# Performance work log

Hardware: AMD Instinct MI355X
Metric: run time of the kernel (lower is better)

## Reference

```python
import jax, jax.numpy as jnp
import numpy as np

OUT_H, OUT_W = 7, 7
SPATIAL_SCALE = 0.125
SAMPLING_RATIO = 2


def setup_inputs() -> dict:
    key = jax.random.key(0)
    k1, k2, k3, k4 = jax.random.split(key, 4)
    inputs = jax.random.normal(k1, (2, 100, 100, 256), dtype=jnp.float32)
    # boxes in image coords (stride-8 feature over ~800px image): x0,y0,x1,y1
    xy0 = jax.random.uniform(k2, (1024, 2), minval=0.0, maxval=600.0)
    wh = jax.random.uniform(k3, (1024, 2), minval=8.0, maxval=200.0)
    boxes = jnp.concatenate([xy0, xy0 + wh], axis=1).astype(jnp.float32)
    box_inds = jax.random.randint(k4, (1024,), 0, 2, dtype=jnp.int32)
    return {"inputs": inputs, "boxes": boxes, "box_inds": box_inds}


def _roi_align(inputs, boxes, box_inds):
    """aligned=True ROIAlign: crop_and_resize at oversampled grid + avg pool.

    Sample coordinate (per aligned=True transform + tf.crop_and_resize):
      x_j = x0*scale + spacing_w*(j+0.5) - 0.5, spacing_w = w_box*scale/crop_w
    Out-of-range samples get extrapolation_value=0 (TF semantics).
    """
    N, H, W, C = inputs.shape
    B = boxes.shape[0]
    ch, cw = OUT_H * SAMPLING_RATIO, OUT_W * SAMPLING_RATIO

    sb = boxes * SPATIAL_SCALE
    x0, y0, x1, y1 = sb[:, 0], sb[:, 1], sb[:, 2], sb[:, 3]
    sw = (x1 - x0) / cw  # [B]
    sh = (y1 - y0) / ch
    xs = x0[:, None] + sw[:, None] * (jnp.arange(cw, dtype=sb.dtype) + 0.5) - 0.5  # [B,cw]
    ys = y0[:, None] + sh[:, None] * (jnp.arange(ch, dtype=sb.dtype) + 0.5) - 0.5  # [B,ch]

    yl = jnp.floor(ys)
    xl = jnp.floor(xs)
    ty = ys - yl  # [B,ch]
    tx = xs - xl  # [B,cw]
    yli = jnp.clip(yl, 0, H - 1).astype(jnp.int32)
    yhi = jnp.clip(yl + 1, 0, H - 1).astype(jnp.int32)
    xli = jnp.clip(xl, 0, W - 1).astype(jnp.int32)
    xhi = jnp.clip(xl + 1, 0, W - 1).astype(jnp.int32)

    b = box_inds[:, None, None]

    def g(yy, xx):  # gather -> [B,ch,cw,C]
        return inputs[b, yy[:, :, None], xx[:, None, :], :]

    txe = tx[:, None, :, None]
    top = g(yli, xli) * (1.0 - txe) + g(yli, xhi) * txe
    bot = g(yhi, xli) * (1.0 - txe) + g(yhi, xhi) * txe
    tye = ty[:, :, None, None]
    out = top * (1.0 - tye) + bot * tye  # [B,ch,cw,C]

    valid = ((ys >= 0) & (ys <= H - 1))[:, :, None] & ((xs >= 0) & (xs <= W - 1))[:, None, :]
    out = jnp.where(valid[..., None], out, 0.0)

    # avg_pool2d kernel=stride=SAMPLING_RATIO (SAME==VALID since exact multiple)
    out = out.reshape(B, OUT_H, SAMPLING_RATIO, OUT_W, SAMPLING_RATIO, C).mean(axis=(2, 4))
    return out  # [B, OUT_H, OUT_W, C]


def reference(inputs, boxes, box_inds):
    return _roi_align(inputs, boxes, box_inds)
```

## Files before the change

### kernel.cpp

```cpp
#include <hip/hip_runtime.h>


constexpr int   H_IN  = 100;
constexpr int   W_IN  = 100;
constexpr int   C_IN  = 256;
constexpr int   OUT_H = 7;
constexpr int   OUT_W = 7;
constexpr int   SR    = 2;
constexpr int   NPIX  = OUT_H * OUT_W;
constexpr int   NBOX  = 1024;
constexpr float SCALE = 0.125f;

typedef float f32x4 __attribute__((ext_vector_type(4)));

__global__ __launch_bounds__(1024) void sort_boxes_kernel(
    const float* __restrict__ boxes,
    const int*   __restrict__ box_inds,
    int*         __restrict__ perm)
{
    const int tid  = threadIdx.x;
    const int wave = tid >> 6;
    const int lane = tid & 63;

    const float y0 = boxes[tid * 4 + 1] * SCALE;
    const float y1 = boxes[tid * 4 + 3] * SCALE;
    const float cy = 0.5f * (y0 + y1);
    int band = (int)(cy * (1.0f / 25.0f));
    band = min(max(band, 0), 3);
    const int bin = box_inds[tid] * 4 + band;

    __shared__ int whist[16][8];
    __shared__ int wbase[16][8];

    int wrank = 0;
    const unsigned long long ltmask = (lane == 63) ? ~0ull >> 1
                                                   : (1ull << lane) - 1;
#pragma unroll
    for (int k = 0; k < 8; ++k) {
        const unsigned long long bal = __ballot(bin == k);
        if (bin == k) wrank = __popcll(bal & ltmask);
        if (lane == 0) whist[wave][k] = __popcll(bal);
    }
    __syncthreads();

    if (tid == 0) {
        int acc = 0;
        for (int k = 0; k < 8; ++k)
            for (int w = 0; w < 16; ++w) {
                wbase[w][k] = acc;
                acc += whist[w][k];
            }
    }
    __syncthreads();

    perm[wbase[wave][bin] + wrank] = tid;
}

template<int NR, int NC>
__device__ __forceinline__ f32x4 gather(const float* __restrict__ base,
                                        const int* ro, const int* co,
                                        const float* wr, const float* wc,
                                        int c4)
{
    f32x4 v[NR * NC];
#pragma unroll
    for (int i = 0; i < NR; ++i)
#pragma unroll
        for (int j = 0; j < NC; ++j)
            v[i * NC + j] = *(const f32x4*)(base + (size_t)((ro[i] + co[j]) * C_IN + c4));

    f32x4 acc = {0.f, 0.f, 0.f, 0.f};
#pragma unroll
    for (int i = 0; i < NR; ++i)
#pragma unroll
        for (int j = 0; j < NC; ++j)
            acc += v[i * NC + j] * (wr[i] * wc[j]);
    return acc;
}

__device__ __forceinline__ int merge_dim(float s0, float s1, int LIM,
                                         int* idx, float* w)
{
    const float f0 = floorf(s0);
    const float f1 = floorf(s1);
    const float t0 = s0 - f0;
    const float t1 = s1 - f1;
    const float va = (s0 >= 0.0f && s0 <= (float)(LIM - 1)) ? 1.0f : 0.0f;
    const float vb = (s1 >= 0.0f && s1 <= (float)(LIM - 1)) ? 1.0f : 0.0f;
    const int i0 = (int)f0;
    const int i1 = (int)f1;

    int n;
    if (i1 == i0) {
        n = 2;
        idx[0] = i0;     w[0] = va * (1.0f - t0) + vb * (1.0f - t1);
        idx[1] = i0 + 1; w[1] = va * t0 + vb * t1;
    } else if (i1 == i0 + 1) {
        n = 3;
        idx[0] = i0;     w[0] = va * (1.0f - t0);
        idx[1] = i0 + 1; w[1] = va * t0 + vb * (1.0f - t1);
        idx[2] = i0 + 2; w[2] = vb * t1;
    } else {
        n = 4;
        idx[0] = i0;     w[0] = va * (1.0f - t0);
        idx[1] = i0 + 1; w[1] = va * t0;
        idx[2] = i1;     w[2] = vb * (1.0f - t1);
        idx[3] = i1 + 1; w[3] = vb * t1;
    }
#pragma unroll
    for (int k = 0; k < 4; ++k)
        idx[k] = min(max(idx[k], 0), LIM - 1);
    return n;
}

__global__ __launch_bounds__(256) void roi_align_kernel(
    const float* __restrict__ inputs,
    const float* __restrict__ boxes,
    const int*   __restrict__ box_inds,
    const int*   __restrict__ perm,
    float*       __restrict__ out)
{
    const int tid  = threadIdx.x;
    const int lane = tid & 63;
    const int sub  = tid >> 6;

    const int nchunk = gridDim.x >> 3;
    const int lbid   = (blockIdx.x & 7) * nchunk + (blockIdx.x >> 3);
    const int p      = lbid * 4 + sub;

    const int bs  = p / NPIX;
    const int b   = perm[bs];
    const int rem = p - bs * NPIX;
    const int oy  = rem / OUT_W;
    const int ox  = rem - oy * OUT_W;

    const float x0 = boxes[b * 4 + 0] * SCALE;
    const float y0 = boxes[b * 4 + 1] * SCALE;
    const float x1 = boxes[b * 4 + 2] * SCALE;
    const float y1 = boxes[b * 4 + 3] * SCALE;
    const float sw = (x1 - x0) * (1.0f / (OUT_W * SR));
    const float sh = (y1 - y0) * (1.0f / (OUT_H * SR));
    const int   n  = box_inds[b];

    const float* base = inputs + (size_t)n * (H_IN * W_IN * C_IN);
    const int c4 = lane * 4;

    const float ys0 = y0 + sh * ((float)(oy * SR) + 0.5f) - 0.5f;
    const float ys1 = ys0 + sh;
    int   ridx[4]; float wr[4];
    const int nr = merge_dim(ys0, ys1, H_IN, ridx, wr);
#pragma unroll
    for (int k = 0; k < 4; ++k) ridx[k] *= W_IN;

    const float xs0 = x0 + sw * ((float)(ox * SR) + 0.5f) - 0.5f;
    const float xs1 = xs0 + sw;
    int   cidx[4]; float wc[4];
    const int nc = merge_dim(xs0, xs1, W_IN, cidx, wc);

    const int sel = __builtin_amdgcn_readfirstlane((nr - 2) * 3 + (nc - 2));

    f32x4 acc;
    switch (sel) {
        case 0: acc = gather<2, 2>(base, ridx, cidx, wr, wc, c4); break;
        case 1: acc = gather<2, 3>(base, ridx, cidx, wr, wc, c4); break;
        case 2: acc = gather<2, 4>(base, ridx, cidx, wr, wc, c4); break;
        case 3: acc = gather<3, 2>(base, ridx, cidx, wr, wc, c4); break;
        case 4: acc = gather<3, 3>(base, ridx, cidx, wr, wc, c4); break;
        case 5: acc = gather<3, 4>(base, ridx, cidx, wr, wc, c4); break;
        case 6: acc = gather<4, 2>(base, ridx, cidx, wr, wc, c4); break;
        case 7: acc = gather<4, 3>(base, ridx, cidx, wr, wc, c4); break;
        default: acc = gather<4, 4>(base, ridx, cidx, wr, wc, c4); break;
    }

    acc *= 0.25f;

    float* op = out + (size_t)b * (NPIX * C_IN) + (size_t)rem * C_IN + c4;
    __builtin_nontemporal_store(acc, (f32x4*)op);
}

extern "C" void kernel_launch(void* const* d_in, const int* in_sizes, int n_in,
                              void* d_out, int out_size, void* d_ws, size_t ws_size,
                              hipStream_t stream) {
    const float* inputs   = (const float*)d_in[0];
    const float* boxes    = (const float*)d_in[1];
    const int*   box_inds = (const int*)d_in[2];
    float*       out      = (float*)d_out;
    int*         perm     = (int*)d_ws;

    sort_boxes_kernel<<<1, NBOX, 0, stream>>>(boxes, box_inds, perm);

    const int npix_total = NBOX * NPIX;
    const int blocks     = npix_total / 4;
    roi_align_kernel<<<blocks, 256, 0, stream>>>(inputs, boxes, box_inds, perm, out);
}
```

Measured before the change: 31.78 us.

## Process half a box per block with shared per-row/column sample tables

Each block now handles half of one box (about 25 output pixels) rather than 4 arbitrary pixels. Fourteen threads compute the row and column offsets and weights once into LDS, and each wave then loops over its pixels. This removes the redundant per-pixel box loads and merge_dim work and cuts the grid from about 12.5K blocks to 2048. The trade-off is fewer blocks, a __syncthreads, and per-wave loops of uneven length, which may hurt latency hiding on the gather loads.

```diff
diff --git a/kernel.cpp b/kernel.cpp
--- a/kernel.cpp
+++ b/kernel.cpp
@@ -6,7 +6,6 @@
 constexpr int   C_IN  = 256;
 constexpr int   OUT_H = 7;
 constexpr int   OUT_W = 7;
-constexpr int   SR    = 2;
 constexpr int   NPIX  = OUT_H * OUT_W;
 constexpr int   NBOX  = 1024;
 constexpr float SCALE = 0.125f;
@@ -54,28 +53,6 @@
     __syncthreads();
 
     perm[wbase[wave][bin] + wrank] = tid;
-}
-
-template<int NR, int NC>
-__device__ __forceinline__ f32x4 gather(const float* __restrict__ base,
-                                        const int* ro, const int* co,
-                                        const float* wr, const float* wc,
-                                        int c4)
-{
-    f32x4 v[NR * NC];
-#pragma unroll
-    for (int i = 0; i < NR; ++i)
-#pragma unroll
-        for (int j = 0; j < NC; ++j)
-            v[i * NC + j] = *(const f32x4*)(base + (size_t)((ro[i] + co[j]) * C_IN + c4));
-
-    f32x4 acc = {0.f, 0.f, 0.f, 0.f};
-#pragma unroll
-    for (int i = 0; i < NR; ++i)
-#pragma unroll
-        for (int j = 0; j < NC; ++j)
-            acc += v[i * NC + j] * (wr[i] * wc[j]);
-    return acc;
 }
 
 __device__ __forceinline__ int merge_dim(float s0, float s1, int LIM,
@@ -95,11 +72,14 @@
         n = 2;
         idx[0] = i0;     w[0] = va * (1.0f - t0) + vb * (1.0f - t1);
         idx[1] = i0 + 1; w[1] = va * t0 + vb * t1;
+        idx[2] = i0;     w[2] = 0.0f;
+        idx[3] = i0;     w[3] = 0.0f;
     } else if (i1 == i0 + 1) {
         n = 3;
         idx[0] = i0;     w[0] = va * (1.0f - t0);
         idx[1] = i0 + 1; w[1] = va * t0 + vb * (1.0f - t1);
         idx[2] = i0 + 2; w[2] = vb * t1;
+        idx[3] = i0;     w[3] = 0.0f;
     } else {
         n = 4;
         idx[0] = i0;     w[0] = va * (1.0f - t0);
@@ -113,7 +93,29 @@
     return n;
 }
 
-__global__ __launch_bounds__(256) void roi_align_kernel(
+template<int NR, int NC>
+__device__ __forceinline__ f32x4 gather(const float* __restrict__ base,
+                                        const int* ro, const int* co,
+                                        const float* wr, const float* wc,
+                                        int c4)
+{
+    f32x4 v[NR * NC];
+#pragma unroll
+    for (int i = 0; i < NR; ++i)
+#pragma unroll
+        for (int j = 0; j < NC; ++j)
+            v[i * NC + j] = *(const f32x4*)(base + (size_t)(ro[i] + co[j] + c4));
+
+    f32x4 acc = {0.f, 0.f, 0.f, 0.f};
+#pragma unroll
+    for (int i = 0; i < NR; ++i)
+#pragma unroll
+        for (int j = 0; j < NC; ++j)
+            acc += v[i * NC + j] * (wr[i] * wc[j]);
+    return acc;
+}
+
+__global__ __launch_bounds__(256, 4) void roi_align_kernel(
     const float* __restrict__ inputs,
     const float* __restrict__ boxes,
     const int*   __restrict__ box_inds,
@@ -122,60 +124,98 @@
 {
     const int tid  = threadIdx.x;
     const int lane = tid & 63;
-    const int sub  = tid >> 6;
+    const int wv   = tid >> 6;
 
     const int nchunk = gridDim.x >> 3;
     const int lbid   = (blockIdx.x & 7) * nchunk + (blockIdx.x >> 3);
-    const int p      = lbid * 4 + sub;
-
-    const int bs  = p / NPIX;
-    const int b   = perm[bs];
-    const int rem = p - bs * NPIX;
-    const int oy  = rem / OUT_W;
-    const int ox  = rem - oy * OUT_W;
-
-    const float x0 = boxes[b * 4 + 0] * SCALE;
-    const float y0 = boxes[b * 4 + 1] * SCALE;
-    const float x1 = boxes[b * 4 + 2] * SCALE;
-    const float y1 = boxes[b * 4 + 3] * SCALE;
-    const float sw = (x1 - x0) * (1.0f / (OUT_W * SR));
-    const float sh = (y1 - y0) * (1.0f / (OUT_H * SR));
-    const int   n  = box_inds[b];
+    const int bs     = lbid >> 1;
+    const int h      = lbid & 1;
+
+    const int b = __builtin_amdgcn_readfirstlane(perm[bs]);
+    const int n = __builtin_amdgcn_readfirstlane(box_inds[b]);
+
+    __shared__ int4   s_roff[OUT_H];
+    __shared__ float4 s_rw[OUT_H];
+    __shared__ int4   s_coff[OUT_W];
+    __shared__ float4 s_cw[OUT_W];
+    __shared__ int    s_nr[OUT_H];
+    __shared__ int    s_nc[OUT_W];
+
+    if (tid < 14) {
+        const float bx0 = boxes[b * 4 + 0] * SCALE;
+        const float by0 = boxes[b * 4 + 1] * SCALE;
+        const float bx1 = boxes[b * 4 + 2] * SCALE;
+        const float by1 = boxes[b * 4 + 3] * SCALE;
+        const float sw  = (bx1 - bx0) * (1.0f / 14.0f);
+        const float sh  = (by1 - by0) * (1.0f / 14.0f);
+
+        int   idx[4];
+        float wgt[4];
+        if (tid < 7) {
+            const int   oy = tid;
+            const float s0 = by0 + sh * ((float)(oy * 2) + 0.5f) - 0.5f;
+            const int   nr = merge_dim(s0, s0 + sh, H_IN, idx, wgt);
+            int4 off; float4 wq;
+#pragma unroll
+            for (int k = 0; k < 4; ++k) {
+                ((int*)&off)[k]   = idx[k] * (W_IN * C_IN);
+                ((float*)&wq)[k]  = wgt[k] * 0.25f;
+            }
+            s_roff[oy] = off; s_rw[oy] = wq; s_nr[oy] = nr;
+        } else {
+            const int   ox = tid - 7;
+            const float s0 = bx0 + sw * ((float)(ox * 2) + 0.5f) - 0.5f;
+            const int   nc = merge_dim(s0, s0 + sw, W_IN, idx, wgt);
+            int4 off; float4 wq;
+#pragma unroll
+            for (int k = 0; k < 4; ++k) {
+                ((int*)&off)[k]   = idx[k] * C_IN;
+                ((float*)&wq)[k]  = wgt[k];
+            }
+            s_coff[ox] = off; s_cw[ox] = wq; s_nc[ox] = nc;
+        }
+    }
+    __syncthreads();
 
     const float* base = inputs + (size_t)n * (H_IN * W_IN * C_IN);
-    const int c4 = lane * 4;
-
-    const float ys0 = y0 + sh * ((float)(oy * SR) + 0.5f) - 0.5f;
-    const float ys1 = ys0 + sh;
-    int   ridx[4]; float wr[4];
-    const int nr = merge_dim(ys0, ys1, H_IN, ridx, wr);
-#pragma unroll
-    for (int k = 0; k < 4; ++k) ridx[k] *= W_IN;
-
-    const float xs0 = x0 + sw * ((float)(ox * SR) + 0.5f) - 0.5f;
-    const float xs1 = xs0 + sw;
-    int   cidx[4]; float wc[4];
-    const int nc = merge_dim(xs0, xs1, W_IN, cidx, wc);
-
-    const int sel = __builtin_amdgcn_readfirstlane((nr - 2) * 3 + (nc - 2));
-
-    f32x4 acc;
-    switch (sel) {
-        case 0: acc = gather<2, 2>(base, ridx, cidx, wr, wc, c4); break;
-        case 1: acc = gather<2, 3>(base, ridx, cidx, wr, wc, c4); break;
-        case 2: acc = gather<2, 4>(base, ridx, cidx, wr, wc, c4); break;
-        case 3: acc = gather<3, 2>(base, ridx, cidx, wr, wc, c4); break;
-        case 4: acc = gather<3, 3>(base, ridx, cidx, wr, wc, c4); break;
-        case 5: acc = gather<3, 4>(base, ridx, cidx, wr, wc, c4); break;
-        case 6: acc = gather<4, 2>(base, ridx, cidx, wr, wc, c4); break;
-        case 7: acc = gather<4, 3>(base, ridx, cidx, wr, wc, c4); break;
-        default: acc = gather<4, 4>(base, ridx, cidx, wr, wc, c4); break;
-    }
-
-    acc *= 0.25f;
-
-    float* op = out + (size_t)b * (NPIX * C_IN) + (size_t)rem * C_IN + c4;
-    __builtin_nontemporal_store(acc, (f32x4*)op);
+    const int    c4   = lane * 4;
+    const int    start = h * 25;
+    const int    pend  = h ? NPIX : 25;
+
+    for (int k = 0; k < 7; ++k) {
+        const int pix = start + wv + 4 * k;
+        if (pix >= pend) break;
+        const int oy = (pix * 37) >> 8;
+        const int ox = pix - oy * 7;
+
+        int4   roI = s_roff[oy];
+        float4 rwV = s_rw[oy];
+        int4   coI = s_coff[ox];
+        float4 cwV = s_cw[ox];
+        const int* ro   = (const int*)&roI;
+        const float* wr = (const float*)&rwV;
+        const int* co   = (const int*)&coI;
+        const float* wc = (const float*)&cwV;
+
+        const int sel = __builtin_amdgcn_readfirstlane(
+            (s_nr[oy] - 2) * 3 + (s_nc[ox] - 2));
+
+        f32x4 acc;
+        switch (sel) {
+            case 0: acc = gather<2, 2>(base, ro, co, wr, wc, c4); break;
+            case 1: acc = gather<2, 3>(base, ro, co, wr, wc, c4); break;
+            case 2: acc = gather<2, 4>(base, ro, co, wr, wc, c4); break;
+            case 3: acc = gather<3, 2>(base, ro, co, wr, wc, c4); break;
+            case 4: acc = gather<3, 3>(base, ro, co, wr, wc, c4); break;
+            case 5: acc = gather<3, 4>(base, ro, co, wr, wc, c4); break;
+            case 6: acc = gather<4, 2>(base, ro, co, wr, wc, c4); break;
+            case 7: acc = gather<4, 3>(base, ro, co, wr, wc, c4); break;
+            default: acc = gather<4, 4>(base, ro, co, wr, wc, c4); break;
+        }
+
+        float* op = out + ((size_t)b * NPIX + pix) * C_IN + c4;
+        __builtin_nontemporal_store(acc, (f32x4*)op);
+    }
 }
 
 extern "C" void kernel_launch(void* const* d_in, const int* in_sizes, int n_in,
@@ -188,8 +228,5 @@
     int*         perm     = (int*)d_ws;
 
     sort_boxes_kernel<<<1, NBOX, 0, stream>>>(boxes, box_inds, perm);
-
-    const int npix_total = NBOX * NPIX;
-    const int blocks     = npix_total / 4;
-    roi_align_kernel<<<blocks, 256, 0, stream>>>(inputs, boxes, box_inds, perm, out);
-}
+    roi_align_kernel<<<NBOX * 2, 256, 0, stream>>>(inputs, boxes, box_inds, perm, out);
+}
```

Measured after the change: 33.25 us. 4.6% more time.

## Precompute per-box row/column sample offsets and weights in a separate meta kernel

Applied to the files above, without the earlier changes.

Adds a meta_kernel that computes, for each sorted box slot, the 7 row and 7 column merged sample offsets, weights and tap counts, and stores them as 32-byte records in workspace. The main gather kernel then loads two records per output pixel instead of doing box loads, floor, merge and index math per wavefront. Batch offset and the 1/4 average are folded into the row offsets and weights, and the tap count is packed into the low bits of the first offset. This adds a third kernel launch and a workspace round trip in exchange for a leaner gather kernel.

```diff
diff --git a/kernel.cpp b/kernel.cpp
--- a/kernel.cpp
+++ b/kernel.cpp
@@ -6,12 +6,16 @@
 constexpr int   C_IN  = 256;
 constexpr int   OUT_H = 7;
 constexpr int   OUT_W = 7;
-constexpr int   SR    = 2;
 constexpr int   NPIX  = OUT_H * OUT_W;
 constexpr int   NBOX  = 1024;
 constexpr float SCALE = 0.125f;
 
 typedef float f32x4 __attribute__((ext_vector_type(4)));
+
+struct Meta { int4 off; float4 w; };
+
+constexpr int RMETA_OFF = 4096;
+constexpr int CMETA_OFF = 4096 + 7168 * 32;
 
 __global__ __launch_bounds__(1024) void sort_boxes_kernel(
     const float* __restrict__ boxes,
@@ -54,28 +58,6 @@
     __syncthreads();
 
     perm[wbase[wave][bin] + wrank] = tid;
-}
-
-template<int NR, int NC>
-__device__ __forceinline__ f32x4 gather(const float* __restrict__ base,
-                                        const int* ro, const int* co,
-                                        const float* wr, const float* wc,
-                                        int c4)
-{
-    f32x4 v[NR * NC];
-#pragma unroll
-    for (int i = 0; i < NR; ++i)
-#pragma unroll
-        for (int j = 0; j < NC; ++j)
-            v[i * NC + j] = *(const f32x4*)(base + (size_t)((ro[i] + co[j]) * C_IN + c4));
-
-    f32x4 acc = {0.f, 0.f, 0.f, 0.f};
-#pragma unroll
-    for (int i = 0; i < NR; ++i)
-#pragma unroll
-        for (int j = 0; j < NC; ++j)
-            acc += v[i * NC + j] * (wr[i] * wc[j]);
-    return acc;
 }
 
 __device__ __forceinline__ int merge_dim(float s0, float s1, int LIM,
@@ -95,11 +77,14 @@
         n = 2;
         idx[0] = i0;     w[0] = va * (1.0f - t0) + vb * (1.0f - t1);
         idx[1] = i0 + 1; w[1] = va * t0 + vb * t1;
+        idx[2] = i0;     w[2] = 0.0f;
+        idx[3] = i0;     w[3] = 0.0f;
     } else if (i1 == i0 + 1) {
         n = 3;
         idx[0] = i0;     w[0] = va * (1.0f - t0);
         idx[1] = i0 + 1; w[1] = va * t0 + vb * (1.0f - t1);
         idx[2] = i0 + 2; w[2] = vb * t1;
+        idx[3] = i0;     w[3] = 0.0f;
     } else {
         n = 4;
         idx[0] = i0;     w[0] = va * (1.0f - t0);
@@ -113,68 +98,125 @@
     return n;
 }
 
-__global__ __launch_bounds__(256) void roi_align_kernel(
-    const float* __restrict__ inputs,
+__global__ __launch_bounds__(256) void meta_kernel(
     const float* __restrict__ boxes,
     const int*   __restrict__ box_inds,
     const int*   __restrict__ perm,
+    Meta*        __restrict__ rmeta,
+    Meta*        __restrict__ cmeta)
+{
+    const int t = blockIdx.x * 256 + threadIdx.x;
+    if (t >= NBOX * 14) return;
+    const int slot = t / 14;
+    const int d    = t - slot * 14;
+
+    const int b = perm[slot];
+    const int n = box_inds[b];
+
+    const float bx0 = boxes[b * 4 + 0] * SCALE;
+    const float by0 = boxes[b * 4 + 1] * SCALE;
+    const float bx1 = boxes[b * 4 + 2] * SCALE;
+    const float by1 = boxes[b * 4 + 3] * SCALE;
+    const float sw  = (bx1 - bx0) * (1.0f / 14.0f);
+    const float sh  = (by1 - by0) * (1.0f / 14.0f);
+
+    int idx[4]; float wgt[4];
+    Meta m;
+    if (d < 7) {
+        const float s0 = by0 + sh * ((float)(d * 2) + 0.5f) - 0.5f;
+        const int   nr = merge_dim(s0, s0 + sh, H_IN, idx, wgt);
+#pragma unroll
+        for (int k = 0; k < 4; ++k) {
+            ((int*)&m.off)[k]  = n * (H_IN * W_IN * C_IN) + idx[k] * (W_IN * C_IN);
+            ((float*)&m.w)[k]  = wgt[k] * 0.25f;
+        }
+        m.off.x |= (nr - 2);
+        rmeta[slot * 7 + d] = m;
+    } else {
+        const int   ox = d - 7;
+        const float s0 = bx0 + sw * ((float)(ox * 2) + 0.5f) - 0.5f;
+        const int   nc = merge_dim(s0, s0 + sw, W_IN, idx, wgt);
+#pragma unroll
+        for (int k = 0; k < 4; ++k) {
+            ((int*)&m.off)[k]  = idx[k] * C_IN;
+            ((float*)&m.w)[k]  = wgt[k];
+        }
+        m.off.x |= (nc - 2);
+        cmeta[slot * 7 + ox] = m;
+    }
+}
+
+template<int NR, int NC>
+__device__ __forceinline__ f32x4 gather(const float* __restrict__ base,
+                                        const int* ro, const int* co,
+                                        const float* wr, const float* wc,
+                                        int c4)
+{
+    f32x4 v[NR * NC];
+#pragma unroll
+    for (int i = 0; i < NR; ++i)
+#pragma unroll
+        for (int j = 0; j < NC; ++j)
+            v[i * NC + j] = *(const f32x4*)(base + (size_t)(ro[i] + co[j] + c4));
+
+    f32x4 acc = {0.f, 0.f, 0.f, 0.f};
+#pragma unroll
+    for (int i = 0; i < NR; ++i)
+#pragma unroll
+        for (int j = 0; j < NC; ++j)
+            acc += v[i * NC + j] * (wr[i] * wc[j]);
+    return acc;
+}
+
+__global__ __launch_bounds__(256) void roi_align_kernel(
+    const float* __restrict__ inputs,
+    const int*   __restrict__ perm,
+    const Meta*  __restrict__ rmeta,
+    const Meta*  __restrict__ cmeta,
     float*       __restrict__ out)
 {
-    const int tid  = threadIdx.x;
-    const int lane = tid & 63;
-    const int sub  = tid >> 6;
+    const int lane = threadIdx.x & 63;
+    const int sub  = __builtin_amdgcn_readfirstlane(threadIdx.x >> 6);
 
     const int nchunk = gridDim.x >> 3;
     const int lbid   = (blockIdx.x & 7) * nchunk + (blockIdx.x >> 3);
     const int p      = lbid * 4 + sub;
 
     const int bs  = p / NPIX;
-    const int b   = perm[bs];
     const int rem = p - bs * NPIX;
-    const int oy  = rem / OUT_W;
-    const int ox  = rem - oy * OUT_W;
-
-    const float x0 = boxes[b * 4 + 0] * SCALE;
-    const float y0 = boxes[b * 4 + 1] * SCALE;
-    const float x1 = boxes[b * 4 + 2] * SCALE;
-    const float y1 = boxes[b * 4 + 3] * SCALE;
-    const float sw = (x1 - x0) * (1.0f / (OUT_W * SR));
-    const float sh = (y1 - y0) * (1.0f / (OUT_H * SR));
-    const int   n  = box_inds[b];
-
-    const float* base = inputs + (size_t)n * (H_IN * W_IN * C_IN);
+    const int oy  = (rem * 37) >> 8;
+    const int ox  = rem - oy * 7;
+
+    const int b = __builtin_amdgcn_readfirstlane(perm[bs]);
+
+    Meta rm = rmeta[bs * 7 + oy];
+    Meta cm = cmeta[bs * 7 + ox];
+
+    const int sel = __builtin_amdgcn_readfirstlane(
+        (rm.off.x & 3) * 3 + (cm.off.x & 3));
+    rm.off.x &= ~3;
+    cm.off.x &= ~3;
+
+    const int* ro   = (const int*)&rm.off;
+    const float* wr = (const float*)&rm.w;
+    const int* co   = (const int*)&cm.off;
+    const float* wc = (const float*)&cm.w;
     const int c4 = lane * 4;
-
-    const float ys0 = y0 + sh * ((float)(oy * SR) + 0.5f) - 0.5f;
-    const float ys1 = ys0 + sh;
-    int   ridx[4]; float wr[4];
-    const int nr = merge_dim(ys0, ys1, H_IN, ridx, wr);
-#pragma unroll
-    for (int k = 0; k < 4; ++k) ridx[k] *= W_IN;
-
-    const float xs0 = x0 + sw * ((float)(ox * SR) + 0.5f) - 0.5f;
-    const float xs1 = xs0 + sw;
-    int   cidx[4]; float wc[4];
-    const int nc = merge_dim(xs0, xs1, W_IN, cidx, wc);
-
-    const int sel = __builtin_amdgcn_readfirstlane((nr - 2) * 3 + (nc - 2));
 
     f32x4 acc;
     switch (sel) {
-        case 0: acc = gather<2, 2>(base, ridx, cidx, wr, wc, c4); break;
-        case 1: acc = gather<2, 3>(base, ridx, cidx, wr, wc, c4); break;
-        case 2: acc = gather<2, 4>(base, ridx, cidx, wr, wc, c4); break;
-        case 3: acc = gather<3, 2>(base, ridx, cidx, wr, wc, c4); break;
-        case 4: acc = gather<3, 3>(base, ridx, cidx, wr, wc, c4); break;
-        case 5: acc = gather<3, 4>(base, ridx, cidx, wr, wc, c4); break;
-        case 6: acc = gather<4, 2>(base, ridx, cidx, wr, wc, c4); break;
-        case 7: acc = gather<4, 3>(base, ridx, cidx, wr, wc, c4); break;
-        default: acc = gather<4, 4>(base, ridx, cidx, wr, wc, c4); break;
-    }
-
-    acc *= 0.25f;
-
-    float* op = out + (size_t)b * (NPIX * C_IN) + (size_t)rem * C_IN + c4;
+        case 0: acc = gather<2, 2>(inputs, ro, co, wr, wc, c4); break;
+        case 1: acc = gather<2, 3>(inputs, ro, co, wr, wc, c4); break;
+        case 2: acc = gather<2, 4>(inputs, ro, co, wr, wc, c4); break;
+        case 3: acc = gather<3, 2>(inputs, ro, co, wr, wc, c4); break;
+        case 4: acc = gather<3, 3>(inputs, ro, co, wr, wc, c4); break;
+        case 5: acc = gather<3, 4>(inputs, ro, co, wr, wc, c4); break;
+        case 6: acc = gather<4, 2>(inputs, ro, co, wr, wc, c4); break;
+        case 7: acc = gather<4, 3>(inputs, ro, co, wr, wc, c4); break;
+        default: acc = gather<4, 4>(inputs, ro, co, wr, wc, c4); break;
+    }
+
+    float* op = out + ((size_t)b * NPIX + rem) * C_IN + c4;
     __builtin_nontemporal_store(acc, (f32x4*)op);
 }
 
@@ -185,11 +227,14 @@
     const float* boxes    = (const float*)d_in[1];
     const int*   box_inds = (const int*)d_in[2];
     float*       out      = (float*)d_out;
-    int*         perm     = (int*)d_ws;
+
+    int*  perm  = (int*)d_ws;
+    Meta* rmeta = (Meta*)((char*)d_ws + RMETA_OFF);
+    Meta* cmeta = (Meta*)((char*)d_ws + CMETA_OFF);
 
     sort_boxes_kernel<<<1, NBOX, 0, stream>>>(boxes, box_inds, perm);
-
-    const int npix_total = NBOX * NPIX;
-    const int blocks     = npix_total / 4;
-    roi_align_kernel<<<blocks, 256, 0, stream>>>(inputs, boxes, box_inds, perm, out);
-}
+    meta_kernel<<<56, 256, 0, stream>>>(boxes, box_inds, perm, rmeta, cmeta);
+
+    const int blocks = NBOX * NPIX / 4;
+    roi_align_kernel<<<blocks, 256, 0, stream>>>(inputs, perm, rmeta, cmeta, out);
+}
```

Result: no change. 31.16 us (-2.0%).
